# Kernel optimization log

Measured on AMD Instinct MI355X. Metric: run time of the kernel, lower is better.

Reference implementation:

```python
import jax, jax.numpy as jnp
import numpy as np

N_ATOMS, N_NBH, N_IN, N_FILTERS, N_OUT, N_GAUSS = 10000, 48, 128, 128, 128, 25
R_CUTOFF = 5.0
LOG2 = float(np.log(2.0))


def ssp(v):
    # shifted softplus, the SchNet activation
    return jax.nn.softplus(v) - LOG2


def setup_inputs() -> dict:
    key = jax.random.key(0)
    ks = jax.random.split(key, 10)
    x = jax.random.normal(ks[0], (N_ATOMS, N_IN), dtype=jnp.float32)
    dR = jax.random.uniform(ks[1], (N_ATOMS, N_NBH), dtype=jnp.float32) * 10.0  # distances in [0,10)
    dR_expanded = jax.random.normal(ks[2], (N_ATOMS, N_NBH, N_GAUSS), dtype=jnp.float32)
    pairwise_mask = jnp.ones((N_ATOMS, N_NBH), dtype=jnp.float32)
    neighbors_idx = jax.random.randint(ks[3], (N_ATOMS, N_NBH), 0, N_ATOMS, dtype=jnp.int32)
    s = 1.0 / np.sqrt(N_FILTERS)
    W1 = jax.random.normal(ks[4], (N_GAUSS, N_FILTERS), dtype=jnp.float32) * (1.0 / np.sqrt(N_GAUSS))
    b1 = jnp.zeros((N_FILTERS,), dtype=jnp.float32)
    W2 = jax.random.normal(ks[5], (N_FILTERS, N_FILTERS), dtype=jnp.float32) * s
    b2 = jnp.zeros((N_FILTERS,), dtype=jnp.float32)
    W_in2f = jax.random.normal(ks[6], (N_IN, N_FILTERS), dtype=jnp.float32) * (1.0 / np.sqrt(N_IN))
    W_f2out = jax.random.normal(ks[7], (N_FILTERS, N_OUT), dtype=jnp.float32) * s
    b_f2out = jnp.zeros((N_OUT,), dtype=jnp.float32)
    return {"x": x, "dR": dR, "dR_expanded": dR_expanded, "pairwise_mask": pairwise_mask,
            "neighbors_idx": neighbors_idx, "W1": W1, "b1": b1, "W2": W2, "b2": b2,
            "W_in2f": W_in2f, "W_f2out": W_f2out, "b_f2out": b_f2out}


def reference(x, dR, dR_expanded, pairwise_mask, neighbors_idx,
              W1, b1, W2, b2, W_in2f, W_f2out, b_f2out):
    # FilterNetwork: Dense + ssp + Dense, on Gaussian-smeared distances -> [N, K, F]
    W = jnp.einsum('nkg,gf->nkf', dR_expanded, W1) + b1
    W = jnp.einsum('nkf,fh->nkh', ssp(W), W2) + b2
    # HardCutoff: 1 where within cutoff
    C = (dR <= R_CUTOFF).astype(W.dtype)           # [N, K]
    W = W * C[..., None]
    # in2f (no bias), gather neighbor features
    y = x @ W_in2f                                  # [N, F]
    y = jnp.take(y, neighbors_idx, axis=0)          # [N, K, F] (gather == take_along_axis path)
    # filter-weighted multiply + masked sum aggregation over neighbor axis
    y = y * W
    y = jnp.sum(y * pairwise_mask[..., None], axis=1)  # [N, F]
    # f2out: Linear + shifted softplus
    return ssp(y @ W_f2out + b_f2out)               # [N, n_out]
```

## Files before the change

### kernel.cpp

```cpp
#include <hip/hip_runtime.h>
#include <hip/hip_bf16.h>


#define NA 10000
#define NK 48
#define NF 128
#define HP  136
#define YFP 136

typedef __bf16 bf16x8 __attribute__((ext_vector_type(8)));
typedef float  f32x4  __attribute__((ext_vector_type(4)));

__device__ __forceinline__ unsigned short f2bs(float x) {
    return __builtin_bit_cast(unsigned short, (__bf16)x);
}
__device__ __forceinline__ float bs2f(unsigned short u) {
    return (float)__builtin_bit_cast(__bf16, u);
}
__device__ __forceinline__ float sspf(float v) {
    return fmaxf(v, 0.0f) + __logf(1.0f + __expf(-fabsf(v))) - 0.69314718056f;
}

__global__ __launch_bounds__(256) void in2f_prep(
    const float* __restrict__ x,
    const float* __restrict__ Wi,
    const float* __restrict__ W1,
    const float* __restrict__ W2,
    const float* __restrict__ Wo,
    unsigned short* __restrict__ wsb,
    unsigned short* __restrict__ yfeatb)
{
    const int tid = threadIdx.x;

    if (blockIdx.x >= 157) {
        int i = (blockIdx.x - 157) * 256 + tid;
        if (i < 4096) {
            int f = i >> 5, g = i & 31;
            wsb[i] = (g < 25) ? f2bs(W1[g * NF + f]) : (unsigned short)0;
        } else if (i < 20480) {
            int j = i - 4096; int h = j >> 7, k = j & 127;
            wsb[i] = f2bs(W2[k * NF + h]);
        } else {
            int j = i - 20480; int f = j >> 7, k = j & 127;
            wsb[i] = f2bs(Wo[k * NF + f]);
        }
        return;
    }

    __shared__ __align__(16) unsigned short s_wi[NF * 136];
    {
        const float4* wi4 = (const float4*)Wi;
        #pragma unroll
        for (int it = 0; it < 16; ++it) {
            int idx4 = it * 256 + tid;
            float4 v = wi4[idx4];
            int i = idx4 >> 5;
            int f = (idx4 & 31) * 4;
            s_wi[(f + 0) * 136 + i] = f2bs(v.x);
            s_wi[(f + 1) * 136 + i] = f2bs(v.y);
            s_wi[(f + 2) * 136 + i] = f2bs(v.z);
            s_wi[(f + 3) * 136 + i] = f2bs(v.w);
        }
    }
    __syncthreads();

    const int w = tid >> 6;
    const int lane = tid & 63;
    const int r = lane & 15;
    const int q = lane >> 4;
    const int m0 = blockIdx.x * 64 + w * 16;
    const int row = m0 + r;
    const bool rv = (row < NA);

    f32x4 acc[8];
    #pragma unroll
    for (int nt = 0; nt < 8; ++nt) { acc[nt][0]=0.f; acc[nt][1]=0.f; acc[nt][2]=0.f; acc[nt][3]=0.f; }

    #pragma unroll
    for (int ks = 0; ks < 4; ++ks) {
        bf16x8 a;
        if (rv) {
            const float4* xp = (const float4*)(x + (size_t)row * NF + ks * 32 + q * 8);
            float4 v0 = xp[0], v1 = xp[1];
            a[0]=(__bf16)v0.x; a[1]=(__bf16)v0.y; a[2]=(__bf16)v0.z; a[3]=(__bf16)v0.w;
            a[4]=(__bf16)v1.x; a[5]=(__bf16)v1.y; a[6]=(__bf16)v1.z; a[7]=(__bf16)v1.w;
        } else {
            #pragma unroll
            for (int j = 0; j < 8; ++j) a[j] = (__bf16)0.0f;
        }
        #pragma unroll
        for (int nt = 0; nt < 8; ++nt) {
            bf16x8 b = *(const bf16x8*)(&s_wi[(nt * 16 + r) * 136 + ks * 32 + q * 8]);
            acc[nt] = __builtin_amdgcn_mfma_f32_16x16x32_bf16(a, b, acc[nt], 0, 0, 0);
        }
    }
    #pragma unroll
    for (int nt = 0; nt < 8; ++nt) {
        #pragma unroll
        for (int reg = 0; reg < 4; ++reg) {
            int orow = m0 + q * 4 + reg;
            if (orow < NA)
                yfeatb[(size_t)orow * NF + nt * 16 + r] = f2bs(acc[nt][reg]);
        }
    }
}

__global__ __launch_bounds__(512) void cfconv_mfma(
    const float* __restrict__ dR,
    const float* __restrict__ dRe,
    const float* __restrict__ mask,
    const int*   __restrict__ nbr,
    const float* __restrict__ b1,
    const float* __restrict__ b2,
    const unsigned short* __restrict__ W1T,
    const unsigned short* __restrict__ W2T,
    const unsigned short* __restrict__ yfeatb,
    float* __restrict__ yout)
{
    __shared__ __align__(16) unsigned short s_H[2][NK * HP];
    __shared__ __align__(16) unsigned short s_yf[2][NK * YFP];
    __shared__ float s_cm[2][NK];

    const int tid = threadIdx.x;
    const int a = tid >> 8;
    const int t8 = tid & 255;
    const int n = blockIdx.x * 2 + a;
    const int w = t8 >> 6;
    const int lane = tid & 63;
    const int r = lane & 15;
    const int q = lane >> 4;
    const int nt0 = w * 2;

    const int kb = t8 >> 4;
    const int sp = t8 & 15;
    const int nb0 = nbr[n * NK + kb] * NF;
    const int nb1 = nbr[n * NK + kb + 16] * NF;
    const int nb2 = nbr[n * NK + kb + 32] * NF;
    bf16x8 g0 = *(const bf16x8*)(yfeatb + nb0 + sp * 8);
    bf16x8 g1 = *(const bf16x8*)(yfeatb + nb1 + sp * 8);
    bf16x8 g2 = *(const bf16x8*)(yfeatb + nb2 + sp * 8);

    bf16x8 bfr0 = *(const bf16x8*)(W1T + ((nt0    ) * 16 + r) * 32 + q * 8);
    bf16x8 bfr1 = *(const bf16x8*)(W1T + ((nt0 + 1) * 16 + r) * 32 + q * 8);
    bf16x8 bw[2][4];
    #pragma unroll
    for (int t = 0; t < 2; ++t)
        #pragma unroll
        for (int ks = 0; ks < 4; ++ks)
            bw[t][ks] = *(const bf16x8*)(W2T + ((nt0 + t) * 16 + r) * NF + ks * 32 + q * 8);

    if (t8 < NK) {
        float d = dR[n * NK + t8];
        float m = mask[n * NK + t8];
        s_cm[a][t8] = (d <= 5.0f) ? m : 0.0f;
    }

    const float bias1a = b1[nt0 * 16 + r];
    const float bias1b = b1[nt0 * 16 + 16 + r];
    const float bias2a = b2[nt0 * 16 + r];
    const float bias2b = b2[nt0 * 16 + 16 + r];

    const float* dre_n = dRe + (size_t)n * (NK * 25);
    #pragma unroll
    for (int mt = 0; mt < 3; ++mt) {
        bf16x8 av8;
        if (q < 3) {
            float av[8];
            __builtin_memcpy(av, dre_n + (mt * 16 + r) * 25 + q * 8, 32);
            #pragma unroll
            for (int j = 0; j < 8; ++j) av8[j] = (__bf16)av[j];
        } else {
            float v = dre_n[(mt * 16 + r) * 25 + 24];
            av8[0] = (__bf16)v;
            #pragma unroll
            for (int j = 1; j < 8; ++j) av8[j] = (__bf16)0.0f;
        }
        f32x4 zf; zf[0]=0.f; zf[1]=0.f; zf[2]=0.f; zf[3]=0.f;
        f32x4 h0v = __builtin_amdgcn_mfma_f32_16x16x32_bf16(av8, bfr0, zf, 0, 0, 0);
        f32x4 h1v = __builtin_amdgcn_mfma_f32_16x16x32_bf16(av8, bfr1, zf, 0, 0, 0);
        #pragma unroll
        for (int reg = 0; reg < 4; ++reg) {
            int k = mt * 16 + q * 4 + reg;
            s_H[a][k * HP + nt0 * 16 + r]      = f2bs(sspf(h0v[reg] + bias1a));
            s_H[a][k * HP + nt0 * 16 + 16 + r] = f2bs(sspf(h1v[reg] + bias1b));
        }
    }

    *(bf16x8*)(&s_yf[a][(kb     ) * YFP + sp * 8]) = g0;
    *(bf16x8*)(&s_yf[a][(kb + 16) * YFP + sp * 8]) = g1;
    *(bf16x8*)(&s_yf[a][(kb + 32) * YFP + sp * 8]) = g2;

    __syncthreads();

    f32x4 acc[3][2];
    #pragma unroll
    for (int mt = 0; mt < 3; ++mt)
        #pragma unroll
        for (int t = 0; t < 2; ++t) { acc[mt][t][0]=0.f; acc[mt][t][1]=0.f; acc[mt][t][2]=0.f; acc[mt][t][3]=0.f; }

    #pragma unroll
    for (int ks = 0; ks < 4; ++ks) {
        #pragma unroll
        for (int mt = 0; mt < 3; ++mt) {
            bf16x8 ah = *(const bf16x8*)(&s_H[a][(mt * 16 + r) * HP + ks * 32 + q * 8]);
            acc[mt][0] = __builtin_amdgcn_mfma_f32_16x16x32_bf16(ah, bw[0][ks], acc[mt][0], 0, 0, 0);
            acc[mt][1] = __builtin_amdgcn_mfma_f32_16x16x32_bf16(ah, bw[1][ks], acc[mt][1], 0, 0, 0);
        }
    }

    float part0 = 0.f, part1 = 0.f;
    const int h0 = nt0 * 16 + r;
    #pragma unroll
    for (int mt = 0; mt < 3; ++mt) {
        #pragma unroll
        for (int reg = 0; reg < 4; ++reg) {
            int k = mt * 16 + q * 4 + reg;
            float cmk = s_cm[a][k];
            part0 += cmk * (acc[mt][0][reg] + bias2a) * bs2f(s_yf[a][k * YFP + h0]);
            part1 += cmk * (acc[mt][1][reg] + bias2b) * bs2f(s_yf[a][k * YFP + h0 + 16]);
        }
    }
    part0 += __shfl_xor(part0, 16);
    part0 += __shfl_xor(part0, 32);
    part1 += __shfl_xor(part1, 16);
    part1 += __shfl_xor(part1, 32);
    if (q == 0) {
        yout[(size_t)n * NF + h0]      = part0;
        yout[(size_t)n * NF + h0 + 16] = part1;
    }
}

__global__ __launch_bounds__(256) void f2out_mfma(
    const unsigned short* __restrict__ WoT,
    const float* __restrict__ bo,
    float* io)
{
    const int tid = threadIdx.x;
    const int w = tid >> 6;
    const int lane = tid & 63;
    const int r = lane & 15;
    const int q = lane >> 4;
    const int m0 = blockIdx.x * 64 + w * 16;
    const int row = m0 + r;
    const bool rv = (row < NA);

    f32x4 acc[8];
    #pragma unroll
    for (int nt = 0; nt < 8; ++nt) { acc[nt][0]=0.f; acc[nt][1]=0.f; acc[nt][2]=0.f; acc[nt][3]=0.f; }

    #pragma unroll
    for (int ks = 0; ks < 4; ++ks) {
        bf16x8 a;
        if (rv) {
            const float4* yp = (const float4*)(io + (size_t)row * NF + ks * 32 + q * 8);
            float4 v0 = yp[0], v1 = yp[1];
            a[0]=(__bf16)v0.x; a[1]=(__bf16)v0.y; a[2]=(__bf16)v0.z; a[3]=(__bf16)v0.w;
            a[4]=(__bf16)v1.x; a[5]=(__bf16)v1.y; a[6]=(__bf16)v1.z; a[7]=(__bf16)v1.w;
        } else {
            #pragma unroll
            for (int j = 0; j < 8; ++j) a[j] = (__bf16)0.0f;
        }
        #pragma unroll
        for (int nt = 0; nt < 8; ++nt) {
            bf16x8 b = *(const bf16x8*)(WoT + (nt * 16 + r) * NF + ks * 32 + q * 8);
            acc[nt] = __builtin_amdgcn_mfma_f32_16x16x32_bf16(a, b, acc[nt], 0, 0, 0);
        }
    }
    #pragma unroll
    for (int nt = 0; nt < 8; ++nt) {
        float bia = bo[nt * 16 + r];
        #pragma unroll
        for (int reg = 0; reg < 4; ++reg) {
            int orow = m0 + q * 4 + reg;
            if (orow < NA)
                io[(size_t)orow * NF + nt * 16 + r] = sspf(acc[nt][reg] + bia);
        }
    }
}

extern "C" void kernel_launch(void* const* d_in, const int* in_sizes, int n_in,
                              void* d_out, int out_size, void* d_ws, size_t ws_size,
                              hipStream_t stream)
{
    const float* x    = (const float*)d_in[0];
    const float* dR   = (const float*)d_in[1];
    const float* dRe  = (const float*)d_in[2];
    const float* mask = (const float*)d_in[3];
    const int*   nbr  = (const int*)d_in[4];
    const float* W1   = (const float*)d_in[5];
    const float* b1   = (const float*)d_in[6];
    const float* W2   = (const float*)d_in[7];
    const float* b2   = (const float*)d_in[8];
    const float* Wi2f = (const float*)d_in[9];
    const float* Wf2o = (const float*)d_in[10];
    const float* bf2o = (const float*)d_in[11];
    float* out = (float*)d_out;

    unsigned short* wsb = (unsigned short*)d_ws;
    unsigned short* W1T    = wsb;
    unsigned short* W2T    = wsb + 4096;
    unsigned short* WoT    = wsb + 20480;
    unsigned short* yfeatb = wsb + 36864;

    in2f_prep<<<301, 256, 0, stream>>>(x, Wi2f, W1, W2, Wf2o, wsb, yfeatb);
    cfconv_mfma<<<NA / 2, 512, 0, stream>>>(dR, dRe, mask, nbr, b1, b2,
                                            W1T, W2T, yfeatb, out);
    f2out_mfma<<<157, 256, 0, stream>>>(WoT, bf2o, out);
}
```

Baseline: 211.2 us.

## Pre-convert dR_expanded to padded bf16 and fuse f2out into cfconv kernel

When the workspace is large enough, the prep kernel gets extra blocks that convert the Gaussian-expanded distances to a 32-wide padded bf16 layout. A new per-atom cfconv kernel then loads MFMA A-fragments directly from that buffer and also performs the f2out linear and shifted softplus, so the separate output kernel is dropped. The fallback path splits the two-atom 512-thread block into one-atom 256-thread blocks. The cost is an extra full read and write pass over dR_expanded in the prep kernel, plus a workspace-size-dependent branch.

Measured after the change: 225.8 us. 6.9% more time.

```diff
diff --git a/kernel.cpp b/kernel.cpp
--- a/kernel.cpp
+++ b/kernel.cpp
@@ -27,10 +27,36 @@
     const float* __restrict__ W1,
     const float* __restrict__ W2,
     const float* __restrict__ Wo,
+    const float* __restrict__ dRe,
     unsigned short* __restrict__ wsb,
-    unsigned short* __restrict__ yfeatb)
+    unsigned short* __restrict__ yfeatb,
+    unsigned short* __restrict__ dreb)
 {
     const int tid = threadIdx.x;
+
+    if (blockIdx.x >= 301) {
+        const float4* src = (const float4*)dRe;
+        for (int j = (blockIdx.x - 301) * 256 + tid; j < 3000000; j += 768 * 256) {
+            float4 v = src[j];
+            int n  = j / 300;
+            int rm = j - n * 300;
+            int i  = rm * 4;
+            int k  = i / 25;
+            int g  = i - k * 25;
+            unsigned short* dst = dreb + (size_t)n * 1536;
+            float vv[4] = {v.x, v.y, v.z, v.w};
+            #pragma unroll
+            for (int e = 0; e < 4; ++e) {
+                dst[k * 32 + g] = f2bs(vv[e]);
+                if (++g == 25) {
+                    #pragma unroll
+                    for (int p = 25; p < 32; ++p) dst[k * 32 + p] = 0;
+                    g = 0; ++k;
+                }
+            }
+        }
+        return;
+    }
 
     if (blockIdx.x >= 157) {
         int i = (blockIdx.x - 157) * 256 + tid;
@@ -105,7 +131,151 @@
     }
 }
 
-__global__ __launch_bounds__(512) void cfconv_mfma(
+__global__ __launch_bounds__(256) void cfconv_direct(
+    const float* __restrict__ dR,
+    const float* __restrict__ mask,
+    const int*   __restrict__ nbr,
+    const float* __restrict__ b1,
+    const float* __restrict__ b2,
+    const float* __restrict__ bf2o,
+    const unsigned short* __restrict__ W1T,
+    const unsigned short* __restrict__ W2T,
+    const unsigned short* __restrict__ WoT,
+    const unsigned short* __restrict__ dreb,
+    const unsigned short* __restrict__ yfeatb,
+    float* __restrict__ out)
+{
+    __shared__ __align__(16) unsigned short s_H[NK * HP];
+    __shared__ __align__(16) unsigned short s_yf[NK * YFP];
+    __shared__ __align__(16) unsigned short s_yb[NF];
+    __shared__ float s_cm[NK];
+
+    const int tid = threadIdx.x;
+    const int n = blockIdx.x;
+    const int w = tid >> 6;
+    const int lane = tid & 63;
+    const int r = lane & 15;
+    const int q = lane >> 4;
+    const int nt0 = w * 2;
+
+    const int kb = tid >> 4;
+    const int sp = tid & 15;
+    const int nb0 = nbr[n * NK + kb] * NF;
+    const int nb1 = nbr[n * NK + kb + 16] * NF;
+    const int nb2 = nbr[n * NK + kb + 32] * NF;
+    bf16x8 g0 = *(const bf16x8*)(yfeatb + nb0 + sp * 8);
+    bf16x8 g1 = *(const bf16x8*)(yfeatb + nb1 + sp * 8);
+    bf16x8 g2 = *(const bf16x8*)(yfeatb + nb2 + sp * 8);
+
+    const unsigned short* dn = dreb + (size_t)n * 1536;
+    bf16x8 a0 = *(const bf16x8*)(dn + (      r) * 32 + q * 8);
+    bf16x8 a1 = *(const bf16x8*)(dn + (16  + r) * 32 + q * 8);
+    bf16x8 a2 = *(const bf16x8*)(dn + (32  + r) * 32 + q * 8);
+
+    bf16x8 bfr0 = *(const bf16x8*)(W1T + ((nt0    ) * 16 + r) * 32 + q * 8);
+    bf16x8 bfr1 = *(const bf16x8*)(W1T + ((nt0 + 1) * 16 + r) * 32 + q * 8);
+    bf16x8 bw[2][4];
+    #pragma unroll
+    for (int t = 0; t < 2; ++t)
+        #pragma unroll
+        for (int ks = 0; ks < 4; ++ks)
+            bw[t][ks] = *(const bf16x8*)(W2T + ((nt0 + t) * 16 + r) * NF + ks * 32 + q * 8);
+
+    if (tid < NK) {
+        float d = dR[n * NK + tid];
+        float m = mask[n * NK + tid];
+        s_cm[tid] = (d <= 5.0f) ? m : 0.0f;
+    }
+
+    const float bias1a = b1[nt0 * 16 + r];
+    const float bias1b = b1[nt0 * 16 + 16 + r];
+    const float bias2a = b2[nt0 * 16 + r];
+    const float bias2b = b2[nt0 * 16 + 16 + r];
+
+    #pragma unroll
+    for (int mt = 0; mt < 3; ++mt) {
+        bf16x8 av8 = (mt == 0) ? a0 : (mt == 1) ? a1 : a2;
+        f32x4 zf; zf[0]=0.f; zf[1]=0.f; zf[2]=0.f; zf[3]=0.f;
+        f32x4 h0v = __builtin_amdgcn_mfma_f32_16x16x32_bf16(av8, bfr0, zf, 0, 0, 0);
+        f32x4 h1v = __builtin_amdgcn_mfma_f32_16x16x32_bf16(av8, bfr1, zf, 0, 0, 0);
+        #pragma unroll
+        for (int reg = 0; reg < 4; ++reg) {
+            int k = mt * 16 + q * 4 + reg;
+            s_H[k * HP + nt0 * 16 + r]      = f2bs(sspf(h0v[reg] + bias1a));
+            s_H[k * HP + nt0 * 16 + 16 + r] = f2bs(sspf(h1v[reg] + bias1b));
+        }
+    }
+
+    *(bf16x8*)(&s_yf[(kb     ) * YFP + sp * 8]) = g0;
+    *(bf16x8*)(&s_yf[(kb + 16) * YFP + sp * 8]) = g1;
+    *(bf16x8*)(&s_yf[(kb + 32) * YFP + sp * 8]) = g2;
+
+    __syncthreads();
+
+    bf16x8 wo[2][4];
+    #pragma unroll
+    for (int t = 0; t < 2; ++t)
+        #pragma unroll
+        for (int ks = 0; ks < 4; ++ks)
+            wo[t][ks] = *(const bf16x8*)(WoT + ((nt0 + t) * 16 + r) * NF + ks * 32 + q * 8);
+    const float bo0 = bf2o[nt0 * 16 + r];
+    const float bo1 = bf2o[nt0 * 16 + 16 + r];
+
+    f32x4 acc[3][2];
+    #pragma unroll
+    for (int mt = 0; mt < 3; ++mt)
+        #pragma unroll
+        for (int t = 0; t < 2; ++t) { acc[mt][t][0]=0.f; acc[mt][t][1]=0.f; acc[mt][t][2]=0.f; acc[mt][t][3]=0.f; }
+
+    #pragma unroll
+    for (int ks = 0; ks < 4; ++ks) {
+        #pragma unroll
+        for (int mt = 0; mt < 3; ++mt) {
+            bf16x8 ah = *(const bf16x8*)(&s_H[(mt * 16 + r) * HP + ks * 32 + q * 8]);
+            acc[mt][0] = __builtin_amdgcn_mfma_f32_16x16x32_bf16(ah, bw[0][ks], acc[mt][0], 0, 0, 0);
+            acc[mt][1] = __builtin_amdgcn_mfma_f32_16x16x32_bf16(ah, bw[1][ks], acc[mt][1], 0, 0, 0);
+        }
+    }
+
+    float part0 = 0.f, part1 = 0.f;
+    const int h0 = nt0 * 16 + r;
+    #pragma unroll
+    for (int mt = 0; mt < 3; ++mt) {
+        #pragma unroll
+        for (int reg = 0; reg < 4; ++reg) {
+            int k = mt * 16 + q * 4 + reg;
+            float cmk = s_cm[k];
+            part0 += cmk * (acc[mt][0][reg] + bias2a) * bs2f(s_yf[k * YFP + h0]);
+            part1 += cmk * (acc[mt][1][reg] + bias2b) * bs2f(s_yf[k * YFP + h0 + 16]);
+        }
+    }
+    part0 += __shfl_xor(part0, 16);
+    part0 += __shfl_xor(part0, 32);
+    part1 += __shfl_xor(part1, 16);
+    part1 += __shfl_xor(part1, 32);
+    if (q == 0) {
+        s_yb[h0]      = f2bs(part0);
+        s_yb[h0 + 16] = f2bs(part1);
+    }
+    __syncthreads();
+
+    f32x4 acco0, acco1;
+    acco0[0]=0.f; acco0[1]=0.f; acco0[2]=0.f; acco0[3]=0.f;
+    acco1[0]=0.f; acco1[1]=0.f; acco1[2]=0.f; acco1[3]=0.f;
+    #pragma unroll
+    for (int ks = 0; ks < 4; ++ks) {
+        bf16x8 ya = *(const bf16x8*)(&s_yb[ks * 32 + q * 8]);
+        acco0 = __builtin_amdgcn_mfma_f32_16x16x32_bf16(ya, wo[0][ks], acco0, 0, 0, 0);
+        acco1 = __builtin_amdgcn_mfma_f32_16x16x32_bf16(ya, wo[1][ks], acco1, 0, 0, 0);
+    }
+    if (q == 0) {
+        out[(size_t)n * NF + h0]      = sspf(acco0[0] + bo0);
+        out[(size_t)n * NF + h0 + 16] = sspf(acco1[0] + bo1);
+    }
+}
+
+
+__global__ __launch_bounds__(256) void cfconv_r4(
     const float* __restrict__ dR,
     const float* __restrict__ dRe,
     const float* __restrict__ mask,
@@ -117,22 +287,20 @@
     const unsigned short* __restrict__ yfeatb,
     float* __restrict__ yout)
 {
-    __shared__ __align__(16) unsigned short s_H[2][NK * HP];
-    __shared__ __align__(16) unsigned short s_yf[2][NK * YFP];
-    __shared__ float s_cm[2][NK];
+    __shared__ __align__(16) unsigned short s_H[NK * HP];
+    __shared__ __align__(16) unsigned short s_yf[NK * YFP];
+    __shared__ float s_cm[NK];
 
     const int tid = threadIdx.x;
-    const int a = tid >> 8;
-    const int t8 = tid & 255;
-    const int n = blockIdx.x * 2 + a;
-    const int w = t8 >> 6;
+    const int n = blockIdx.x;
+    const int w = tid >> 6;
     const int lane = tid & 63;
     const int r = lane & 15;
     const int q = lane >> 4;
     const int nt0 = w * 2;
 
-    const int kb = t8 >> 4;
-    const int sp = t8 & 15;
+    const int kb = tid >> 4;
+    const int sp = tid & 15;
     const int nb0 = nbr[n * NK + kb] * NF;
     const int nb1 = nbr[n * NK + kb + 16] * NF;
     const int nb2 = nbr[n * NK + kb + 32] * NF;
@@ -149,10 +317,10 @@
         for (int ks = 0; ks < 4; ++ks)
             bw[t][ks] = *(const bf16x8*)(W2T + ((nt0 + t) * 16 + r) * NF + ks * 32 + q * 8);
 
-    if (t8 < NK) {
-        float d = dR[n * NK + t8];
-        float m = mask[n * NK + t8];
-        s_cm[a][t8] = (d <= 5.0f) ? m : 0.0f;
+    if (tid < NK) {
+        float d = dR[n * NK + tid];
+        float m = mask[n * NK + tid];
+        s_cm[tid] = (d <= 5.0f) ? m : 0.0f;
     }
 
     const float bias1a = b1[nt0 * 16 + r];
@@ -181,14 +349,14 @@
         #pragma unroll
         for (int reg = 0; reg < 4; ++reg) {
             int k = mt * 16 + q * 4 + reg;
-            s_H[a][k * HP + nt0 * 16 + r]      = f2bs(sspf(h0v[reg] + bias1a));
-            s_H[a][k * HP + nt0 * 16 + 16 + r] = f2bs(sspf(h1v[reg] + bias1b));
-        }
-    }
-
-    *(bf16x8*)(&s_yf[a][(kb     ) * YFP + sp * 8]) = g0;
-    *(bf16x8*)(&s_yf[a][(kb + 16) * YFP + sp * 8]) = g1;
-    *(bf16x8*)(&s_yf[a][(kb + 32) * YFP + sp * 8]) = g2;
+            s_H[k * HP + nt0 * 16 + r]      = f2bs(sspf(h0v[reg] + bias1a));
+            s_H[k * HP + nt0 * 16 + 16 + r] = f2bs(sspf(h1v[reg] + bias1b));
+        }
+    }
+
+    *(bf16x8*)(&s_yf[(kb     ) * YFP + sp * 8]) = g0;
+    *(bf16x8*)(&s_yf[(kb + 16) * YFP + sp * 8]) = g1;
+    *(bf16x8*)(&s_yf[(kb + 32) * YFP + sp * 8]) = g2;
 
     __syncthreads();
 
@@ -202,7 +370,7 @@
     for (int ks = 0; ks < 4; ++ks) {
         #pragma unroll
         for (int mt = 0; mt < 3; ++mt) {
-            bf16x8 ah = *(const bf16x8*)(&s_H[a][(mt * 16 + r) * HP + ks * 32 + q * 8]);
+            bf16x8 ah = *(const bf16x8*)(&s_H[(mt * 16 + r) * HP + ks * 32 + q * 8]);
             acc[mt][0] = __builtin_amdgcn_mfma_f32_16x16x32_bf16(ah, bw[0][ks], acc[mt][0], 0, 0, 0);
             acc[mt][1] = __builtin_amdgcn_mfma_f32_16x16x32_bf16(ah, bw[1][ks], acc[mt][1], 0, 0, 0);
         }
@@ -215,9 +383,9 @@
         #pragma unroll
         for (int reg = 0; reg < 4; ++reg) {
             int k = mt * 16 + q * 4 + reg;
-            float cmk = s_cm[a][k];
-            part0 += cmk * (acc[mt][0][reg] + bias2a) * bs2f(s_yf[a][k * YFP + h0]);
-            part1 += cmk * (acc[mt][1][reg] + bias2b) * bs2f(s_yf[a][k * YFP + h0 + 16]);
+            float cmk = s_cm[k];
+            part0 += cmk * (acc[mt][0][reg] + bias2a) * bs2f(s_yf[k * YFP + h0]);
+            part1 += cmk * (acc[mt][1][reg] + bias2b) * bs2f(s_yf[k * YFP + h0 + 16]);
         }
     }
     part0 += __shfl_xor(part0, 16);
@@ -301,9 +469,18 @@
     unsigned short* W2T    = wsb + 4096;
     unsigned short* WoT    = wsb + 20480;
     unsigned short* yfeatb = wsb + 36864;
-
-    in2f_prep<<<301, 256, 0, stream>>>(x, Wi2f, W1, W2, Wf2o, wsb, yfeatb);
-    cfconv_mfma<<<NA / 2, 512, 0, stream>>>(dR, dRe, mask, nbr, b1, b2,
-                                            W1T, W2T, yfeatb, out);
-    f2out_mfma<<<157, 256, 0, stream>>>(WoT, bf2o, out);
-}
+    unsigned short* dreb   = wsb + 1316864;
+
+    const bool big = ws_size >= 33353728ULL;
+
+    in2f_prep<<<big ? 1069 : 301, 256, 0, stream>>>(x, Wi2f, W1, W2, Wf2o, dRe,
+                                                    wsb, yfeatb, dreb);
+    if (big) {
+        cfconv_direct<<<NA, 256, 0, stream>>>(dR, mask, nbr, b1, b2, bf2o,
+                                              W1T, W2T, WoT, dreb, yfeatb, out);
+    } else {
+        cfconv_r4<<<NA, 256, 0, stream>>>(dR, dRe, mask, nbr, b1, b2,
+                                          W1T, W2T, yfeatb, out);
+        f2out_mfma<<<157, 256, 0, stream>>>(WoT, bf2o, out);
+    }
+}
```

## Make cfconv kernel persistent, one atom per 256-thread block iteration

Applied to the files above, without the earlier changes.

The cfconv kernel now launches 1250 blocks of 256 threads that loop over atoms in a grid-stride loop, one atom per iteration. Before, it launched 5000 blocks of 512 threads, each handling two atoms. The W1/W2 weight fragments and biases are loaded into registers once per block and reused across about eight atoms, which removes repeated weight loads and block launch overhead. In exchange, each iteration has two barriers and no overlap of the gather and dRe loads with compute inside a block, so latency hiding depends on several blocks being resident per CU.

New measurement: 202.5 us. 1.04x faster.

```diff
diff --git a/kernel.cpp b/kernel.cpp
--- a/kernel.cpp
+++ b/kernel.cpp
@@ -105,7 +105,7 @@
     }
 }
 
-__global__ __launch_bounds__(512) void cfconv_mfma(
+__global__ __launch_bounds__(256) void cfconv_p(
     const float* __restrict__ dR,
     const float* __restrict__ dRe,
     const float* __restrict__ mask,
@@ -117,28 +117,18 @@
     const unsigned short* __restrict__ yfeatb,
     float* __restrict__ yout)
 {
-    __shared__ __align__(16) unsigned short s_H[2][NK * HP];
-    __shared__ __align__(16) unsigned short s_yf[2][NK * YFP];
-    __shared__ float s_cm[2][NK];
+    __shared__ __align__(16) unsigned short s_H[NK * HP];
+    __shared__ __align__(16) unsigned short s_yf[NK * YFP];
+    __shared__ float s_cm[NK];
 
     const int tid = threadIdx.x;
-    const int a = tid >> 8;
-    const int t8 = tid & 255;
-    const int n = blockIdx.x * 2 + a;
-    const int w = t8 >> 6;
+    const int w = tid >> 6;
     const int lane = tid & 63;
     const int r = lane & 15;
     const int q = lane >> 4;
     const int nt0 = w * 2;
-
-    const int kb = t8 >> 4;
-    const int sp = t8 & 15;
-    const int nb0 = nbr[n * NK + kb] * NF;
-    const int nb1 = nbr[n * NK + kb + 16] * NF;
-    const int nb2 = nbr[n * NK + kb + 32] * NF;
-    bf16x8 g0 = *(const bf16x8*)(yfeatb + nb0 + sp * 8);
-    bf16x8 g1 = *(const bf16x8*)(yfeatb + nb1 + sp * 8);
-    bf16x8 g2 = *(const bf16x8*)(yfeatb + nb2 + sp * 8);
+    const int kb = tid >> 4;
+    const int sp = tid & 15;
 
     bf16x8 bfr0 = *(const bf16x8*)(W1T + ((nt0    ) * 16 + r) * 32 + q * 8);
     bf16x8 bfr1 = *(const bf16x8*)(W1T + ((nt0 + 1) * 16 + r) * 32 + q * 8);
@@ -148,85 +138,95 @@
         #pragma unroll
         for (int ks = 0; ks < 4; ++ks)
             bw[t][ks] = *(const bf16x8*)(W2T + ((nt0 + t) * 16 + r) * NF + ks * 32 + q * 8);
-
-    if (t8 < NK) {
-        float d = dR[n * NK + t8];
-        float m = mask[n * NK + t8];
-        s_cm[a][t8] = (d <= 5.0f) ? m : 0.0f;
-    }
-
     const float bias1a = b1[nt0 * 16 + r];
     const float bias1b = b1[nt0 * 16 + 16 + r];
     const float bias2a = b2[nt0 * 16 + r];
     const float bias2b = b2[nt0 * 16 + 16 + r];
 
-    const float* dre_n = dRe + (size_t)n * (NK * 25);
-    #pragma unroll
-    for (int mt = 0; mt < 3; ++mt) {
-        bf16x8 av8;
-        if (q < 3) {
-            float av[8];
-            __builtin_memcpy(av, dre_n + (mt * 16 + r) * 25 + q * 8, 32);
-            #pragma unroll
-            for (int j = 0; j < 8; ++j) av8[j] = (__bf16)av[j];
-        } else {
-            float v = dre_n[(mt * 16 + r) * 25 + 24];
-            av8[0] = (__bf16)v;
-            #pragma unroll
-            for (int j = 1; j < 8; ++j) av8[j] = (__bf16)0.0f;
-        }
-        f32x4 zf; zf[0]=0.f; zf[1]=0.f; zf[2]=0.f; zf[3]=0.f;
-        f32x4 h0v = __builtin_amdgcn_mfma_f32_16x16x32_bf16(av8, bfr0, zf, 0, 0, 0);
-        f32x4 h1v = __builtin_amdgcn_mfma_f32_16x16x32_bf16(av8, bfr1, zf, 0, 0, 0);
-        #pragma unroll
-        for (int reg = 0; reg < 4; ++reg) {
-            int k = mt * 16 + q * 4 + reg;
-            s_H[a][k * HP + nt0 * 16 + r]      = f2bs(sspf(h0v[reg] + bias1a));
-            s_H[a][k * HP + nt0 * 16 + 16 + r] = f2bs(sspf(h1v[reg] + bias1b));
-        }
-    }
-
-    *(bf16x8*)(&s_yf[a][(kb     ) * YFP + sp * 8]) = g0;
-    *(bf16x8*)(&s_yf[a][(kb + 16) * YFP + sp * 8]) = g1;
-    *(bf16x8*)(&s_yf[a][(kb + 32) * YFP + sp * 8]) = g2;
-
-    __syncthreads();
-
-    f32x4 acc[3][2];
-    #pragma unroll
-    for (int mt = 0; mt < 3; ++mt)
-        #pragma unroll
-        for (int t = 0; t < 2; ++t) { acc[mt][t][0]=0.f; acc[mt][t][1]=0.f; acc[mt][t][2]=0.f; acc[mt][t][3]=0.f; }
-
-    #pragma unroll
-    for (int ks = 0; ks < 4; ++ks) {
+    for (int n = blockIdx.x; n < NA; n += gridDim.x) {
+        const int nb0 = nbr[n * NK + kb] * NF;
+        const int nb1 = nbr[n * NK + kb + 16] * NF;
+        const int nb2 = nbr[n * NK + kb + 32] * NF;
+        bf16x8 g0 = *(const bf16x8*)(yfeatb + nb0 + sp * 8);
+        bf16x8 g1 = *(const bf16x8*)(yfeatb + nb1 + sp * 8);
+        bf16x8 g2 = *(const bf16x8*)(yfeatb + nb2 + sp * 8);
+
+        if (tid < NK) {
+            float d = dR[n * NK + tid];
+            float m = mask[n * NK + tid];
+            s_cm[tid] = (d <= 5.0f) ? m : 0.0f;
+        }
+
+        const float* dre_n = dRe + (size_t)n * (NK * 25);
         #pragma unroll
         for (int mt = 0; mt < 3; ++mt) {
-            bf16x8 ah = *(const bf16x8*)(&s_H[a][(mt * 16 + r) * HP + ks * 32 + q * 8]);
-            acc[mt][0] = __builtin_amdgcn_mfma_f32_16x16x32_bf16(ah, bw[0][ks], acc[mt][0], 0, 0, 0);
-            acc[mt][1] = __builtin_amdgcn_mfma_f32_16x16x32_bf16(ah, bw[1][ks], acc[mt][1], 0, 0, 0);
-        }
-    }
-
-    float part0 = 0.f, part1 = 0.f;
-    const int h0 = nt0 * 16 + r;
-    #pragma unroll
-    for (int mt = 0; mt < 3; ++mt) {
-        #pragma unroll
-        for (int reg = 0; reg < 4; ++reg) {
-            int k = mt * 16 + q * 4 + reg;
-            float cmk = s_cm[a][k];
-            part0 += cmk * (acc[mt][0][reg] + bias2a) * bs2f(s_yf[a][k * YFP + h0]);
-            part1 += cmk * (acc[mt][1][reg] + bias2b) * bs2f(s_yf[a][k * YFP + h0 + 16]);
-        }
-    }
-    part0 += __shfl_xor(part0, 16);
-    part0 += __shfl_xor(part0, 32);
-    part1 += __shfl_xor(part1, 16);
-    part1 += __shfl_xor(part1, 32);
-    if (q == 0) {
-        yout[(size_t)n * NF + h0]      = part0;
-        yout[(size_t)n * NF + h0 + 16] = part1;
+            bf16x8 av8;
+            if (q < 3) {
+                float av[8];
+                __builtin_memcpy(av, dre_n + (mt * 16 + r) * 25 + q * 8, 32);
+                #pragma unroll
+                for (int j = 0; j < 8; ++j) av8[j] = (__bf16)av[j];
+            } else {
+                float v = dre_n[(mt * 16 + r) * 25 + 24];
+                av8[0] = (__bf16)v;
+                #pragma unroll
+                for (int j = 1; j < 8; ++j) av8[j] = (__bf16)0.0f;
+            }
+            f32x4 zf; zf[0]=0.f; zf[1]=0.f; zf[2]=0.f; zf[3]=0.f;
+            f32x4 h0v = __builtin_amdgcn_mfma_f32_16x16x32_bf16(av8, bfr0, zf, 0, 0, 0);
+            f32x4 h1v = __builtin_amdgcn_mfma_f32_16x16x32_bf16(av8, bfr1, zf, 0, 0, 0);
+            #pragma unroll
+            for (int reg = 0; reg < 4; ++reg) {
+                int k = mt * 16 + q * 4 + reg;
+                s_H[k * HP + nt0 * 16 + r]      = f2bs(sspf(h0v[reg] + bias1a));
+                s_H[k * HP + nt0 * 16 + 16 + r] = f2bs(sspf(h1v[reg] + bias1b));
+            }
+        }
+
+        *(bf16x8*)(&s_yf[(kb     ) * YFP + sp * 8]) = g0;
+        *(bf16x8*)(&s_yf[(kb + 16) * YFP + sp * 8]) = g1;
+        *(bf16x8*)(&s_yf[(kb + 32) * YFP + sp * 8]) = g2;
+
+        __syncthreads();
+
+        f32x4 acc[3][2];
+        #pragma unroll
+        for (int mt = 0; mt < 3; ++mt)
+            #pragma unroll
+            for (int t = 0; t < 2; ++t) { acc[mt][t][0]=0.f; acc[mt][t][1]=0.f; acc[mt][t][2]=0.f; acc[mt][t][3]=0.f; }
+
+        #pragma unroll
+        for (int ks = 0; ks < 4; ++ks) {
+            #pragma unroll
+            for (int mt = 0; mt < 3; ++mt) {
+                bf16x8 ah = *(const bf16x8*)(&s_H[(mt * 16 + r) * HP + ks * 32 + q * 8]);
+                acc[mt][0] = __builtin_amdgcn_mfma_f32_16x16x32_bf16(ah, bw[0][ks], acc[mt][0], 0, 0, 0);
+                acc[mt][1] = __builtin_amdgcn_mfma_f32_16x16x32_bf16(ah, bw[1][ks], acc[mt][1], 0, 0, 0);
+            }
+        }
+
+        float part0 = 0.f, part1 = 0.f;
+        const int h0 = nt0 * 16 + r;
+        #pragma unroll
+        for (int mt = 0; mt < 3; ++mt) {
+            #pragma unroll
+            for (int reg = 0; reg < 4; ++reg) {
+                int k = mt * 16 + q * 4 + reg;
+                float cmk = s_cm[k];
+                part0 += cmk * (acc[mt][0][reg] + bias2a) * bs2f(s_yf[k * YFP + h0]);
+                part1 += cmk * (acc[mt][1][reg] + bias2b) * bs2f(s_yf[k * YFP + h0 + 16]);
+            }
+        }
+        part0 += __shfl_xor(part0, 16);
+        part0 += __shfl_xor(part0, 32);
+        part1 += __shfl_xor(part1, 16);
+        part1 += __shfl_xor(part1, 32);
+        if (q == 0) {
+            yout[(size_t)n * NF + h0]      = part0;
+            yout[(size_t)n * NF + h0 + 16] = part1;
+        }
+
+        __syncthreads();
     }
 }
 
@@ -303,7 +303,7 @@
     unsigned short* yfeatb = wsb + 36864;
 
     in2f_prep<<<301, 256, 0, stream>>>(x, Wi2f, W1, W2, Wf2o, wsb, yfeatb);
-    cfconv_mfma<<<NA / 2, 512, 0, stream>>>(dR, dRe, mask, nbr, b1, b2,
-                                            W1T, W2T, yfeatb, out);
+    cfconv_p<<<1250, 256, 0, stream>>>(dR, dRe, mask, nbr, b1, b2,
+                                       W1T, W2T, yfeatb, out);
     f2out_mfma<<<157, 256, 0, stream>>>(WoT, bf2o, out);
 }
```
